# Kernel tuning notes

Measured on AMD Instinct MI355X. Metric: run time of the kernel, lower is better.

The kernel has to match this reference:

```python
import jax, jax.numpy as jnp
import numpy as np

N = 16384      # total ligand atoms
E = 65536      # edges
B = 256        # graphs / batch
MAXN = 64      # atoms per graph (max_nodes for to_dense_batch)
FIN = 64       # num_node_features
HID = 256      # hidden_channels
GH = 2         # gat heads
LP = 1024      # protein length
NH = 4         # cross-attention heads
HD = HID // NH
VOCAB = 22


def setup_inputs() -> dict:
    key = jax.random.key(0)
    ks = jax.random.split(key, 48)
    f = jnp.float32
    def nrm(k, shape, s=0.05):
        return jax.random.normal(k, shape, f) * s
    inp = {}
    inp["x"] = jax.random.normal(ks[0], (N, FIN), f)
    inp["edge_index"] = jax.random.randint(ks[1], (2, E), 0, N)
    inp["batch"] = jnp.arange(N) // MAXN  # sorted, 64 atoms per graph
    inp["protein_seq"] = jax.random.randint(ks[2], (B, LP), 0, VOCAB)
    # GAT layer 1 (FIN -> HID, GH heads, concat=False)
    inp["w1"] = nrm(ks[3], (FIN, GH * HID)); inp["as1"] = nrm(ks[4], (GH, HID)); inp["ad1"] = nrm(ks[5], (GH, HID)); inp["b1"] = jnp.zeros((HID,), f)
    inp["w2"] = nrm(ks[6], (HID, GH * HID)); inp["as2"] = nrm(ks[7], (GH, HID)); inp["ad2"] = nrm(ks[8], (GH, HID)); inp["b2"] = jnp.zeros((HID,), f)
    inp["w3"] = nrm(ks[9], (HID, GH * HID)); inp["as3"] = nrm(ks[10], (GH, HID)); inp["ad3"] = nrm(ks[11], (GH, HID)); inp["b3"] = jnp.zeros((HID,), f)
    # protein embedding + conv1d (OIH layout)
    inp["emb"] = nrm(ks[12], (VOCAB, HID), 0.1)
    inp["conv_w"] = nrm(ks[13], (HID, HID, 3)); inp["conv_b"] = jnp.zeros((HID,), f)
    # cross-attention MHA
    inp["wq"] = nrm(ks[14], (HID, HID)); inp["bq"] = jnp.zeros((HID,), f)
    inp["wk"] = nrm(ks[15], (HID, HID)); inp["bk"] = jnp.zeros((HID,), f)
    inp["wv"] = nrm(ks[16], (HID, HID)); inp["bv"] = jnp.zeros((HID,), f)
    inp["wo"] = nrm(ks[17], (HID, HID)); inp["bo"] = jnp.zeros((HID,), f)
    inp["ln1_g"] = jnp.ones((HID,), f); inp["ln1_b"] = jnp.zeros((HID,), f)
    inp["ffw1"] = nrm(ks[18], (HID, 4 * HID)); inp["ffb1"] = jnp.zeros((4 * HID,), f)
    inp["ffw2"] = nrm(ks[19], (4 * HID, HID)); inp["ffb2"] = jnp.zeros((HID,), f)
    inp["ln2_g"] = jnp.ones((HID,), f); inp["ln2_b"] = jnp.zeros((HID,), f)
    inp["fc1_w"] = nrm(ks[20], (HID, HID)); inp["fc1_b"] = jnp.zeros((HID,), f)
    inp["fc2_w"] = nrm(ks[21], (HID, 1)); inp["fc2_b"] = jnp.zeros((1,), f)
    return inp


def _gat(x, edge_index, W, a_src, a_dst, bias):
    # PyG GATConv, concat=False (mean over heads), add_self_loops=True
    n = x.shape[0]
    h = (x @ W).reshape(n, GH, HID)                      # [N,GH,C]
    loop = jnp.arange(n)
    src = jnp.concatenate([edge_index[0], loop])
    dst = jnp.concatenate([edge_index[1], loop])
    a_s = jnp.einsum('nhc,hc->nh', h, a_src)             # [N,GH]
    a_d = jnp.einsum('nhc,hc->nh', h, a_dst)
    e = jax.nn.leaky_relu(a_s[src] + a_d[dst], 0.2)      # [E+N,GH]
    emax = jax.ops.segment_max(e, dst, num_segments=n)   # each node has a self-loop
    ex = jnp.exp(e - emax[dst])
    den = jax.ops.segment_sum(ex, dst, num_segments=n)
    alpha = ex / den[dst]                                # [E+N,GH]
    msg = h[src] * alpha[:, :, None]
    out = jax.ops.segment_sum(msg, dst, num_segments=n)  # [N,GH,C]
    return out.mean(axis=1) + bias


def _to_dense_batch(x, batch):
    # batch is sorted node->graph ids; counts per graph <= MAXN
    ones = jnp.ones((x.shape[0],), jnp.int32)
    counts = jax.ops.segment_sum(ones, batch, num_segments=B)
    starts = jnp.cumsum(counts) - counts
    pos = jnp.arange(x.shape[0]) - starts[batch]
    dense = jnp.zeros((B, MAXN, x.shape[1]), x.dtype).at[batch, pos].set(x)
    mask = jnp.zeros((B, MAXN), bool).at[batch, pos].set(True)
    return dense, mask


def _layernorm(x, g, b, eps=1e-5):
    mu = x.mean(-1, keepdims=True)
    var = ((x - mu) ** 2).mean(-1, keepdims=True)
    return (x - mu) * jax.lax.rsqrt(var + eps) * g + b


def reference(x, edge_index, batch, protein_seq,
              w1, as1, ad1, b1, w2, as2, ad2, b2, w3, as3, ad3, b3,
              emb, conv_w, conv_b,
              wq, bq, wk, bk, wv, bv, wo, bo,
              ln1_g, ln1_b, ffw1, ffb1, ffw2, ffb2, ln2_g, ln2_b,
              fc1_w, fc1_b, fc2_w, fc2_b):
    # --- ligand GNN (eval mode: dropout = identity) ---
    h = jax.nn.elu(_gat(x, edge_index, w1, as1, ad1, b1))
    h = jax.nn.elu(_gat(h, edge_index, w2, as2, ad2, b2))
    h = jax.nn.elu(_gat(h, edge_index, w3, as3, ad3, b3))
    lig, lig_mask = _to_dense_batch(h, batch)            # [B,MAXN,HID], [B,MAXN]
    # --- protein branch ---
    p = emb[protein_seq]                                 # [B,LP,HID]
    p = p.transpose(0, 2, 1)                             # [B,HID,LP]
    p = jax.lax.conv_general_dilated(p, conv_w, (1,), [(1, 1)],
                                     dimension_numbers=('NCH', 'OIH', 'NCH'))
    p = jax.nn.relu(p + conv_b[None, :, None]).transpose(0, 2, 1)  # [B,LP,HID]
    kpm = protein_seq == 0                               # key padding mask
    # --- cross attention (query=ligand, key/value=protein) ---
    q = (lig @ wq + bq).reshape(B, MAXN, NH, HD)
    k = (p @ wk + bk).reshape(B, LP, NH, HD)
    v = (p @ wv + bv).reshape(B, LP, NH, HD)
    scores = jnp.einsum('bqhd,bkhd->bhqk', q, k) / np.sqrt(HD).astype(np.float32)
    scores = jnp.where(kpm[:, None, None, :], jnp.float32(-1e9), scores)
    attn = jax.nn.softmax(scores, axis=-1)               # [B,NH,MAXN,LP]
    ctx = jnp.einsum('bhqk,bkhd->bqhd', attn, v).reshape(B, MAXN, HID)
    attn_out = ctx @ wo + bo
    y = _layernorm(lig + attn_out, ln1_g, ln1_b)
    ff = jax.nn.gelu(y @ ffw1 + ffb1, approximate=False) @ ffw2 + ffb2
    y = _layernorm(y + ff, ln2_g, ln2_b)
    # --- masked mean pool ---
    m = lig_mask[:, :, None].astype(y.dtype)
    pooled = (y * m).sum(axis=1) / (m.sum(axis=1) + 1e-6)
    out = jax.nn.relu(pooled @ fc1_w + fc1_b)
    return out @ fc2_w + fc2_b                           # [B,1]
```

## Files before the change

kernel.cpp:

```cpp
#include <hip/hip_runtime.h>
#include <hip/hip_bf16.h>
#include <cstdint>
#include <cstddef>

#define NAT 16384
#define NED 65536
#define BGR 256
#define FIN 64
#define HID 256
#define LPN 1024
#define HD 64
#define NTRIP 11638
#define NTAB  11648

typedef __bf16 bf16x8 __attribute__((ext_vector_type(8)));
typedef float floatx4 __attribute__((ext_vector_type(4)));

__device__ __forceinline__ void gl2lds16(const void* g, void* l)
{
    __builtin_amdgcn_global_load_lds(
        (const __attribute__((address_space(1))) unsigned int*)g,
        (__attribute__((address_space(3))) unsigned int*)l, 16, 0, 0);
}

template<int ACT, int OUTBF16, int BIASROW, int HSPLIT>
__global__ __launch_bounds__(512) void gemm_mfma(const __bf16* __restrict__ A,
    const __bf16* __restrict__ Bt, const float* __restrict__ bias,
    void* __restrict__ Cout, int M, int Nn, int K, float escale)
{
    __shared__ __bf16 As[2][128][32];
    __shared__ __bf16 Bs[2][128][32];
    const int t = threadIdx.x;
    const int m0 = blockIdx.y * 128, n0 = blockIdx.x * 128;
    const int w = t >> 6, lane = t & 63;
    const int wm = (w & 3) * 32, wn = (w >> 2) * 64;
    const int quad = lane >> 4, l16 = lane & 15;
    const int r0 = t >> 2, s0 = t & 3, g0 = (s0 ^ (r0 & 3)) * 8;
    const int fso = (quad ^ (l16 & 3)) * 8;
    floatx4 acc[2][4] = {};
    for (int k0 = 0; k0 < K; k0 += 64) {
        gl2lds16(A + (size_t)(m0 + r0) * K + k0 + g0,       &As[0][r0][s0 * 8]);
        gl2lds16(A + (size_t)(m0 + r0) * K + k0 + 32 + g0,  &As[1][r0][s0 * 8]);
        gl2lds16(Bt + (size_t)(n0 + r0) * K + k0 + g0,      &Bs[0][r0][s0 * 8]);
        gl2lds16(Bt + (size_t)(n0 + r0) * K + k0 + 32 + g0, &Bs[1][r0][s0 * 8]);
        __syncthreads();
#pragma unroll
        for (int c = 0; c < 2; c++) {
            bf16x8 af[2], bfr[4];
#pragma unroll
            for (int mi = 0; mi < 2; mi++) af[mi]  = *(const bf16x8*)&As[c][wm + mi * 16 + l16][fso];
#pragma unroll
            for (int nj = 0; nj < 4; nj++) bfr[nj] = *(const bf16x8*)&Bs[c][wn + nj * 16 + l16][fso];
#pragma unroll
            for (int mi = 0; mi < 2; mi++)
#pragma unroll
                for (int nj = 0; nj < 4; nj++)
                    acc[mi][nj] = __builtin_amdgcn_mfma_f32_16x16x32_bf16(af[mi], bfr[nj], acc[mi][nj], 0, 0, 0);
        }
        __syncthreads();
    }
#pragma unroll
    for (int mi = 0; mi < 2; mi++)
#pragma unroll
        for (int nj = 0; nj < 4; nj++) {
            int col = n0 + wn + nj * 16 + l16;
#pragma unroll
            for (int r = 0; r < 4; r++) {
                int row = m0 + wm + mi * 16 + quad * 4 + r;
                float bval = bias ? (BIASROW ? bias[row] : bias[col]) : 0.f;
                float v = (acc[mi][nj][r] + bval) * escale;
                if (ACT == 1) v = fmaxf(v, 0.f);
                if (ACT == 2) v = 0.5f * v * (1.f + erff(v * 0.70710678118654752f));
                if (HSPLIT)      ((__bf16*)Cout)[((size_t)(col >> 6) * M + row) * 64 + (col & 63)] = (__bf16)v;
                else if (OUTBF16) ((__bf16*)Cout)[(size_t)row * Nn + col] = (__bf16)v;
                else              ((float*)Cout)[(size_t)row * Nn + col] = v;
            }
        }
}

__global__ __launch_bounds__(512) void gemm_gat(const __bf16* __restrict__ A,
    const __bf16* __restrict__ Bt, const float* __restrict__ as_f,
    const float* __restrict__ ad_f, __bf16* __restrict__ Hg,
    float* __restrict__ part, int K)
{
    __shared__ __bf16 As[2][128][32];
    __shared__ __bf16 Bs[2][128][32];
    const int t = threadIdx.x;
    const int m0 = blockIdx.y * 128, n0 = blockIdx.x * 128;
    const int w = t >> 6, lane = t & 63;
    const int wm = (w & 3) * 32, wn = (w >> 2) * 64;
    const int quad = lane >> 4, l16 = lane & 15;
    const int r0 = t >> 2, s0 = t & 3, g0 = (s0 ^ (r0 & 3)) * 8;
    const int fso = (quad ^ (l16 & 3)) * 8;
    floatx4 acc[2][4] = {};
    for (int k0 = 0; k0 < K; k0 += 64) {
        gl2lds16(A + (size_t)(m0 + r0) * K + k0 + g0,       &As[0][r0][s0 * 8]);
        gl2lds16(A + (size_t)(m0 + r0) * K + k0 + 32 + g0,  &As[1][r0][s0 * 8]);
        gl2lds16(Bt + (size_t)(n0 + r0) * K + k0 + g0,      &Bs[0][r0][s0 * 8]);
        gl2lds16(Bt + (size_t)(n0 + r0) * K + k0 + 32 + g0, &Bs[1][r0][s0 * 8]);
        __syncthreads();
#pragma unroll
        for (int c = 0; c < 2; c++) {
            bf16x8 af[2], bfr[4];
#pragma unroll
            for (int mi = 0; mi < 2; mi++) af[mi]  = *(const bf16x8*)&As[c][wm + mi * 16 + l16][fso];
#pragma unroll
            for (int nj = 0; nj < 4; nj++) bfr[nj] = *(const bf16x8*)&Bs[c][wn + nj * 16 + l16][fso];
#pragma unroll
            for (int mi = 0; mi < 2; mi++)
#pragma unroll
                for (int nj = 0; nj < 4; nj++)
                    acc[mi][nj] = __builtin_amdgcn_mfma_f32_16x16x32_bf16(af[mi], bfr[nj], acc[mi][nj], 0, 0, 0);
        }
        __syncthreads();
    }
    const int slot = blockIdx.x * 2 + (w >> 2);
#pragma unroll
    for (int mi = 0; mi < 2; mi++) {
#pragma unroll
        for (int r = 0; r < 4; r++) {
            float ps = 0.f, pd = 0.f;
#pragma unroll
            for (int nj = 0; nj < 4; nj++) {
                int col = n0 + wn + nj * 16 + l16;
                float v = acc[mi][nj][r];
                ps += v * as_f[col];
                pd += v * ad_f[col];
            }
#pragma unroll
            for (int off = 1; off < 16; off <<= 1) {
                ps += __shfl_xor(ps, off, 64);
                pd += __shfl_xor(pd, off, 64);
            }
            if (l16 == 0) {
                int row = m0 + wm + mi * 16 + quad * 4 + r;
                part[(size_t)(slot * 2 + 0) * NAT + row] = ps;
                part[(size_t)(slot * 2 + 1) * NAT + row] = pd;
            }
        }
    }
#pragma unroll
    for (int mi = 0; mi < 2; mi++)
#pragma unroll
        for (int nj = 0; nj < 4; nj++) {
            int col = n0 + wn + nj * 16 + l16;
#pragma unroll
            for (int r = 0; r < 4; r++) {
                int row = m0 + wm + mi * 16 + quad * 4 + r;
                Hg[(size_t)row * 512 + col] = (__bf16)acc[mi][nj][r];
            }
        }
}

__global__ void fold_k(const float* __restrict__ part, float* __restrict__ a_s,
                       float* __restrict__ a_d)
{
    int n = blockIdx.x * 256 + threadIdx.x;
    float s0 = 0.f, d0 = 0.f, s1 = 0.f, d1 = 0.f;
#pragma unroll
    for (int sl = 0; sl < 4; sl++) {
        s0 += part[(size_t)(sl * 2 + 0) * NAT + n];
        d0 += part[(size_t)(sl * 2 + 1) * NAT + n];
        s1 += part[(size_t)((sl + 4) * 2 + 0) * NAT + n];
        d1 += part[(size_t)((sl + 4) * 2 + 1) * NAT + n];
    }
    a_s[n * 2 + 0] = s0; a_s[n * 2 + 1] = s1;
    a_d[n * 2 + 0] = d0; a_d[n * 2 + 1] = d1;
}

__global__ __launch_bounds__(256) void tap_k(const float* __restrict__ emb,
    const float* __restrict__ cw, float* __restrict__ tap)
{
    const int dlv = blockIdx.x >> 2, part = blockIdx.x & 3;
    const int dl = dlv / 22, v = dlv % 22;
    const int n = threadIdx.x;
    const float* er = emb + v * 256 + part * 64;
    const float* wr = cw + (size_t)n * 768 + part * 192 + dl;
    float s = 0.f;
    for (int k = 0; k < 64; k += 4) {
        s += er[k + 0] * wr[k * 3 + 0];
        s += er[k + 1] * wr[k * 3 + 3];
        s += er[k + 2] * wr[k * 3 + 6];
        s += er[k + 3] * wr[k * 3 + 9];
    }
    atomicAdd(&tap[(size_t)dlv * 256 + n], s);
}

__global__ __launch_bounds__(256) void ptab_k(const float* __restrict__ tap,
    const float* __restrict__ bias, __bf16* __restrict__ P)
{
    const int t = threadIdx.x;
    const int row = blockIdx.x * 8 + (t >> 5);
    const int c = (t & 31) * 8;
    __bf16 o[8];
    if (row < NTRIP) {
        const int a = row / 506, rem = row - a * 506;
        const int t1 = rem / 23, c2 = rem - t1 * 23;
        float acc[8];
#pragma unroll
        for (int j = 0; j < 8; j++) acc[j] = bias[c + j];
        if (a > 0) {
            const float* r = tap + (size_t)(0 * 22 + (a - 1)) * 256 + c;
#pragma unroll
            for (int j = 0; j < 8; j++) acc[j] += r[j];
        }
        {
            const float* r = tap + (size_t)(1 * 22 + t1) * 256 + c;
#pragma unroll
            for (int j = 0; j < 8; j++) acc[j] += r[j];
        }
        if (c2 > 0) {
            const float* r = tap + (size_t)(2 * 22 + (c2 - 1)) * 256 + c;
#pragma unroll
            for (int j = 0; j < 8; j++) acc[j] += r[j];
        }
#pragma unroll
        for (int j = 0; j < 8; j++) o[j] = (__bf16)fmaxf(acc[j], 0.f);
    } else {
#pragma unroll
        for (int j = 0; j < 8; j++) o[j] = (__bf16)0.f;
    }
    *(uint4*)(P + (size_t)row * 256 + c) = *(uint4*)o;
}

__global__ void tid_k(const int* __restrict__ seq, unsigned short* __restrict__ tid)
{
    int i = blockIdx.x * 256 + threadIdx.x;
    int b = i >> 10, l = i & 1023;
    const int* sr = seq + b * LPN;
    int t0 = (l > 0) ? sr[l - 1] : -1;
    int t1 = sr[l];
    int t2 = (l < LPN - 1) ? sr[l + 1] : -1;
    int v = (t0 + 1) * 506 + t1 * 23 + (t2 + 1);
    tid[i] = (unsigned short)(v | (t1 == 0 ? 0x8000 : 0));
}

struct Segs {
    const float* src[12];
    __bf16* dst[12];
    int kdim[12];
    int ndim[12];
    int mode[12];
    int start[13];
};

__global__ void cvtall_k(Segs S, int total)
{
    int i = blockIdx.x * 256 + threadIdx.x;
    if (i >= total) return;
    int s = 0;
    while (i >= S.start[s + 1]) s++;
    int j = i - S.start[s];
    if (S.mode[s] == 0) {
        S.dst[s][j] = (__bf16)S.src[s][j];
    } else {
        int K = S.kdim[s], N = S.ndim[s];
        int n = j / K, k = j - n * K;
        S.dst[s][j] = (__bf16)S.src[s][(size_t)k * N + n];
    }
}

__global__ void deg_k(const int* __restrict__ ei, int* __restrict__ deg)
{
    int e = blockIdx.x * 256 + threadIdx.x;
    if (e < NED) atomicAdd(&deg[ei[NED + e]], 1);
}

__global__ __launch_bounds__(256) void scan_k(const int* __restrict__ deg, int* __restrict__ rowptr)
{
    __shared__ int part[256];
    int t = threadIdx.x;
    int base = t * 64;
    int s = 0;
#pragma unroll
    for (int i = 0; i < 64; i++) s += deg[base + i];
    part[t] = s;
    __syncthreads();
    for (int off = 1; off < 256; off <<= 1) {
        int v = (t >= off) ? part[t - off] : 0;
        __syncthreads();
        part[t] += v;
        __syncthreads();
    }
    int run = t ? part[t - 1] : 0;
    for (int i = 0; i < 64; i++) { rowptr[base + i] = run; run += deg[base + i]; }
    if (t == 255) rowptr[16384] = run;
}

__global__ void scat_k(const int* __restrict__ ei, int* __restrict__ fill,
                       const int* __restrict__ rowptr, int* __restrict__ csrc,
                       int* __restrict__ cdst)
{
    int e = blockIdx.x * 256 + threadIdx.x;
    if (e >= NED) return;
    int d = ei[NED + e];
    int pos = rowptr[d] + atomicAdd(&fill[d], 1);
    csrc[pos] = ei[e];
    cdst[pos] = d;
}

__global__ void erec_k(const int* __restrict__ csrc, const int* __restrict__ cdst,
    const float* __restrict__ a_s, const float* __restrict__ a_d,
    float4* __restrict__ rec)
{
    int p = blockIdx.x * 256 + threadIdx.x;
    if (p >= NED) return;
    int s = csrc[p], d = cdst[p];
    float2 as2 = *(const float2*)(a_s + s * 2);
    float2 ad2 = *(const float2*)(a_d + d * 2);
    float e0 = as2.x + ad2.x; e0 = (e0 > 0.f) ? e0 : 0.2f * e0;
    float e1 = as2.y + ad2.y; e1 = (e1 > 0.f) ? e1 : 0.2f * e1;
    rec[p] = make_float4(e0, e1, __int_as_float(s), 0.f);
}

__global__ __launch_bounds__(256) void gat_agg(const int* __restrict__ rowptr,
    const float4* __restrict__ rec, const __bf16* __restrict__ hgb,
    const float* __restrict__ a_s, const float* __restrict__ a_d,
    const float* __restrict__ bias, float* __restrict__ out, __bf16* __restrict__ outb)
{
    const int wave = threadIdx.x >> 6, lane = threadIdx.x & 63;
    const int d = blockIdx.x * 4 + wave;
    const int beg = rowptr[d], end = rowptr[d + 1];
    float2 as2 = *(const float2*)(a_s + d * 2);
    float2 ad2 = *(const float2*)(a_d + d * 2);
    float e0 = as2.x + ad2.x; e0 = (e0 > 0.f) ? e0 : 0.2f * e0;
    float e1 = as2.y + ad2.y; e1 = (e1 > 0.f) ? e1 : 0.2f * e1;
    float m0 = e0, den0 = 1.f, m1 = e1, den1 = 1.f;
    for (int p = beg; p < end; p++) {
        float4 rc = rec[p];
        float nm0 = fmaxf(m0, rc.x);
        den0 = den0 * __expf(m0 - nm0) + __expf(rc.x - nm0);
        m0 = nm0;
        float nm1 = fmaxf(m1, rc.y);
        den1 = den1 * __expf(m1 - nm1) + __expf(rc.y - nm1);
        m1 = nm1;
    }
    const float inv0 = 1.f / den0, inv1 = 1.f / den1;
    const int ch = lane * 8;
    const int g = ch >> 8;
    const float mg = g ? m1 : m0, invg = g ? inv1 : inv0;
    float acc[8] = {};
    {
        float al = __expf((g ? e1 : e0) - mg) * invg;
        bf16x8 hv = *(const bf16x8*)(hgb + (size_t)d * 512 + ch);
#pragma unroll
        for (int j = 0; j < 8; j++) acc[j] += (float)hv[j] * al;
    }
    for (int p = beg; p < end; p++) {
        float4 rc = rec[p];
        float al = __expf((g ? rc.y : rc.x) - mg) * invg;
        int s = __float_as_int(rc.z);
        bf16x8 hv = *(const bf16x8*)(hgb + (size_t)s * 512 + ch);
#pragma unroll
        for (int j = 0; j < 8; j++) acc[j] += (float)hv[j] * al;
    }
    float other[8];
#pragma unroll
    for (int j = 0; j < 8; j++) other[j] = __shfl_xor(acc[j], 32, 64);
    if (lane < 32) {
#pragma unroll
        for (int j = 0; j < 8; j++) {
            float v = 0.5f * (acc[j] + other[j]) + bias[ch + j];
            v = (v > 0.f) ? v : expm1f(v);
            if (out) out[(size_t)d * 256 + ch + j] = v;
            outb[(size_t)d * 256 + ch + j] = (__bf16)v;
        }
    }
}

__global__ __launch_bounds__(256, 4) void attn5_k(const __bf16* __restrict__ Qb,
    const __bf16* __restrict__ Ktab, const __bf16* __restrict__ Vtab,
    const unsigned short* __restrict__ tid16, __bf16* __restrict__ O)
{
    __shared__ __bf16 Vs[2][4096];
    __shared__ __bf16 Ps2[4][16][64];
    __shared__ float mask_f[1024];
    __shared__ unsigned short tids[1024];
    const int t = threadIdx.x;
    const int bid = blockIdx.x;
    const int h = (bid >> 1) & 3;
    const int b = ((bid >> 3) << 1) | (bid & 1);
    const int w = t >> 6, lane = t & 63;
    const int quad = lane >> 4, l16 = lane & 15;
    const int key = (l16 & 7) << 4;
    const __bf16* Kh = Ktab + (size_t)h * NTAB * 64;
    const __bf16* Vh = Vtab + (size_t)h * NTAB * 64;
    {
        const uint32_t* src = (const uint32_t*)(tid16 + (size_t)b * LPN);
        uint32_t v0 = src[t], v1 = src[t + 256];
        ((uint32_t*)tids)[t] = v0;
        ((uint32_t*)tids)[t + 256] = v1;
        mask_f[2 * t + 0] = (v0 & 0x8000u) ? -1e9f : 0.f;
        mask_f[2 * t + 1] = (v0 & 0x80000000u) ? -1e9f : 0.f;
        mask_f[2 * (t + 256) + 0] = (v1 & 0x8000u) ? -1e9f : 0.f;
        mask_f[2 * (t + 256) + 1] = (v1 & 0x80000000u) ? -1e9f : 0.f;
    }
    const __bf16* qrow = Qb + (size_t)(b * 64 + w * 16 + l16) * HID + h * HD;
    bf16x8 aq0 = *(const bf16x8*)(qrow + quad * 8);
    bf16x8 aq1 = *(const bf16x8*)(qrow + 32 + quad * 8);
    __syncthreads();

    auto loadV = [&](int kt, bf16x8* vr) {
#pragma unroll
        for (int it = 0; it < 2; it++) {
            const int ch0 = (w + it * 4) * 8;
            const int row = tids[kt * 64 + lane] & 0x7fff;
            vr[it] = *(const bf16x8*)(Vh + (size_t)row * 64 + ch0);
        }
    };
    auto writeV = [&](const bf16x8* vr, int buf) {
#pragma unroll
        for (int it = 0; it < 2; it++) {
            const int ch0 = (w + it * 4) * 8;
#pragma unroll
            for (int j = 0; j < 8; j++) {
                const int chl = ch0 + j;
                Vs[buf][chl * 64 + (((lane >> 3) ^ (chl & 7)) << 3) + (lane & 7)] = vr[it][j];
            }
        }
    };

    bf16x8 vr[2];
    loadV(0, vr);
    writeV(vr, 0);
    float m_run = -3e38f;
    float l_run = 0.f;
    floatx4 ctx[4] = {};
    __syncthreads();

    for (int kt = 0; kt < 16; kt++) {
        const int buf = kt & 1;
        const int kp0 = kt * 64;
        bf16x8 kc0[4], kc1[4];
#pragma unroll
        for (int nj = 0; nj < 4; nj++) {
            const int row = tids[kp0 + nj * 16 + l16] & 0x7fff;
            const __bf16* krow = Kh + (size_t)row * 64;
            kc0[nj] = *(const bf16x8*)(krow + quad * 8);
            kc1[nj] = *(const bf16x8*)(krow + 32 + quad * 8);
        }
        if (kt < 15) loadV(kt + 1, vr);
        floatx4 s[4];
#pragma unroll
        for (int nj = 0; nj < 4; nj++) {
            floatx4 z = {0.f, 0.f, 0.f, 0.f};
            s[nj] = __builtin_amdgcn_mfma_f32_16x16x32_bf16(kc0[nj], aq0, z, 0, 0, 0);
            s[nj] = __builtin_amdgcn_mfma_f32_16x16x32_bf16(kc1[nj], aq1, s[nj], 0, 0, 0);
        }
#pragma unroll
        for (int nj = 0; nj < 4; nj++) {
            floatx4 m4 = *(const floatx4*)&mask_f[kp0 + nj * 16 + quad * 4];
#pragma unroll
            for (int r = 0; r < 4; r++) s[nj][r] += m4[r];
        }
        float mx = -3e38f;
#pragma unroll
        for (int nj = 0; nj < 4; nj++)
#pragma unroll
            for (int r = 0; r < 4; r++) mx = fmaxf(mx, s[nj][r]);
        mx = fmaxf(mx, __shfl_xor(mx, 16, 64));
        mx = fmaxf(mx, __shfl_xor(mx, 32, 64));
        const float mn = fmaxf(m_run, mx);
        const float alpha = __expf(m_run - mn);
        m_run = mn;
        float rs = 0.f;
#pragma unroll
        for (int nj = 0; nj < 4; nj++)
#pragma unroll
            for (int r = 0; r < 4; r++) {
                float p = __expf(s[nj][r] - mn);
                s[nj][r] = p;
                rs += p;
            }
        rs += __shfl_xor(rs, 16, 64);
        rs += __shfl_xor(rs, 32, 64);
        l_run = l_run * alpha + rs;
        float al[4];
#pragma unroll
        for (int r = 0; r < 4; r++) al[r] = __shfl(alpha, quad * 4 + r, 64);
        {
            char* rowp = (char*)&Ps2[w][l16][0];
#pragma unroll
            for (int nj = 0; nj < 4; nj++) {
                union { uint2 u2; unsigned short us[4]; } pk;
#pragma unroll
                for (int r = 0; r < 4; r++) {
                    __bf16 bv = (__bf16)s[nj][r];
                    pk.us[r] = *(unsigned short*)&bv;
                }
                *(uint2*)(rowp + ((nj * 32 + quad * 8) ^ key)) = pk.u2;
            }
        }
        bf16x8 pa0 = *(const bf16x8*)((char*)&Ps2[w][l16][0] + ((quad * 16) ^ key));
        bf16x8 pa1 = *(const bf16x8*)((char*)&Ps2[w][l16][0] + ((64 + quad * 16) ^ key));
#pragma unroll
        for (int dj = 0; dj < 4; dj++) {
#pragma unroll
            for (int r = 0; r < 4; r++) ctx[dj][r] *= al[r];
            const int chl = dj * 16 + l16;
            bf16x8 bv0 = *(const bf16x8*)&Vs[buf][chl * 64 + ((quad ^ (chl & 7)) << 3)];
            bf16x8 bv1 = *(const bf16x8*)&Vs[buf][chl * 64 + (((quad + 4) ^ (chl & 7)) << 3)];
            ctx[dj] = __builtin_amdgcn_mfma_f32_16x16x32_bf16(pa0, bv0, ctx[dj], 0, 0, 0);
            ctx[dj] = __builtin_amdgcn_mfma_f32_16x16x32_bf16(pa1, bv1, ctx[dj], 0, 0, 0);
        }
        if (kt < 15) writeV(vr, buf ^ 1);
        __syncthreads();
    }
    float ll[4];
#pragma unroll
    for (int r = 0; r < 4; r++) ll[r] = __shfl(l_run, quad * 4 + r, 64);
#pragma unroll
    for (int dj = 0; dj < 4; dj++)
#pragma unroll
        for (int r = 0; r < 4; r++) {
            int q = w * 16 + quad * 4 + r;
            O[((size_t)(b * 64 + q)) * 256 + h * HD + dj * 16 + l16] = (__bf16)(ctx[dj][r] / ll[r]);
        }
}

__device__ __forceinline__ float blockSum256(float v, float* red)
{
#pragma unroll
    for (int off = 32; off >= 1; off >>= 1) v += __shfl_down(v, off, 64);
    int wave = threadIdx.x >> 6, lane = threadIdx.x & 63;
    if (lane == 0) red[wave] = v;
    __syncthreads();
    float s = red[0] + red[1] + red[2] + red[3];
    __syncthreads();
    return s;
}

__global__ __launch_bounds__(256) void lnres_k(const float* __restrict__ A,
    const float* __restrict__ Bb, const float* __restrict__ g,
    const float* __restrict__ be, float* __restrict__ Y, __bf16* __restrict__ Yb)
{
    __shared__ float red[4];
    int r = blockIdx.x, t = threadIdx.x;
    float v = A[(size_t)r * 256 + t] + Bb[(size_t)r * 256 + t];
    float mean = blockSum256(v, red) * (1.f / 256.f);
    float d = v - mean;
    float var = blockSum256(d * d, red) * (1.f / 256.f);
    float o = d * rsqrtf(var + 1e-5f) * g[t] + be[t];
    Y[(size_t)r * 256 + t] = o;
    if (Yb) Yb[(size_t)r * 256 + t] = (__bf16)o;
}

__global__ __launch_bounds__(256) void head_k(const float* __restrict__ Y,
    const float* __restrict__ fc1w, const float* __restrict__ fc1b,
    const float* __restrict__ fc2w, const float* __restrict__ fc2b,
    float* __restrict__ out)
{
    __shared__ float pooled[256];
    __shared__ float h[256];
    __shared__ float red[4];
    int b = blockIdx.x, t = threadIdx.x;
    float s = 0.f;
#pragma unroll 8
    for (int q = 0; q < 64; q++) s += Y[(size_t)(b * 64 + q) * 256 + t];
    pooled[t] = s / (64.f + 1e-6f);
    __syncthreads();
    float a = 0.f;
    for (int k = 0; k < 256; k += 4) {
        a += pooled[k + 0] * fc1w[(k + 0) * 256 + t];
        a += pooled[k + 1] * fc1w[(k + 1) * 256 + t];
        a += pooled[k + 2] * fc1w[(k + 2) * 256 + t];
        a += pooled[k + 3] * fc1w[(k + 3) * 256 + t];
    }
    h[t] = fmaxf(a + fc1b[t], 0.f);
    __syncthreads();
    float p = h[t] * fc2w[t];
    p = blockSum256(p, red);
    if (t == 0) out[b] = p + fc2b[0];
}

extern "C" void kernel_launch(void* const* d_in, const int* in_sizes, int n_in,
                              void* d_out, int out_size, void* d_ws, size_t ws_size,
                              hipStream_t stream)
{
    const float* x     = (const float*)d_in[0];
    const int*   ei    = (const int*)d_in[1];
    const int*   pseq  = (const int*)d_in[3];
    const float* w1  = (const float*)d_in[4];
    const float* as1 = (const float*)d_in[5];
    const float* ad1 = (const float*)d_in[6];
    const float* b1  = (const float*)d_in[7];
    const float* w2  = (const float*)d_in[8];
    const float* as2 = (const float*)d_in[9];
    const float* ad2 = (const float*)d_in[10];
    const float* b2  = (const float*)d_in[11];
    const float* w3  = (const float*)d_in[12];
    const float* as3 = (const float*)d_in[13];
    const float* ad3 = (const float*)d_in[14];
    const float* b3  = (const float*)d_in[15];
    const float* emb    = (const float*)d_in[16];
    const float* conv_w = (const float*)d_in[17];
    const float* conv_b = (const float*)d_in[18];
    const float* wq = (const float*)d_in[19];
    const float* bq = (const float*)d_in[20];
    const float* wk = (const float*)d_in[21];
    const float* bk = (const float*)d_in[22];
    const float* wv = (const float*)d_in[23];
    const float* bv = (const float*)d_in[24];
    const float* wo = (const float*)d_in[25];
    const float* bo = (const float*)d_in[26];
    const float* ln1_g = (const float*)d_in[27];
    const float* ln1_b = (const float*)d_in[28];
    const float* ffw1  = (const float*)d_in[29];
    const float* ffb1  = (const float*)d_in[30];
    const float* ffw2  = (const float*)d_in[31];
    const float* ffb2  = (const float*)d_in[32];
    const float* ln2_g = (const float*)d_in[33];
    const float* ln2_b = (const float*)d_in[34];
    const float* fc1_w = (const float*)d_in[35];
    const float* fc1_b = (const float*)d_in[36];
    const float* fc2_w = (const float*)d_in[37];
    const float* fc2_b = (const float*)d_in[38];
    (void)in_sizes; (void)n_in; (void)out_size;

    char* ws = (char*)d_ws;
    size_t off = 0;
    auto alloc = [&](size_t bytes) -> char* {
        char* p = ws + off;
        off += (bytes + 255) & ~(size_t)255;
        return p;
    };
    __bf16* hgb  = (__bf16*)alloc((size_t)NAT * 512 * 2);
    float* og    = (float*)alloc((size_t)NAT * 512 * 4);
    float* hb0   = (float*)alloc((size_t)NAT * 256 * 4);
    float* hb1   = (float*)alloc((size_t)NAT * 256 * 4);
    __bf16* xb   = (__bf16*)alloc((size_t)NAT * FIN * 2);
    __bf16* hbb  = (__bf16*)alloc((size_t)NAT * 256 * 2);
    __bf16* qbb  = (__bf16*)alloc((size_t)NAT * 256 * 2);
    __bf16* ctxbb= (__bf16*)alloc((size_t)NAT * 256 * 2);
    __bf16* ybb  = (__bf16*)alloc((size_t)NAT * 256 * 2);
    float* a_s   = (float*)alloc((size_t)NAT * 2 * 4);
    float* a_d   = (float*)alloc((size_t)NAT * 2 * 4);
    float* asd_p = (float*)alloc((size_t)16 * NAT * 4);
    int* deg     = (int*)alloc((size_t)NAT * 4);
    int* fill    = (int*)alloc((size_t)NAT * 4);
    int* rowptr  = (int*)alloc((size_t)(NAT + 1) * 4);
    int* csrc    = (int*)alloc((size_t)NED * 4);
    int* cdst    = (int*)alloc((size_t)NED * 4);
    float4* erec = (float4*)alloc((size_t)NED * 16);
    float* tap   = (float*)alloc((size_t)3 * 22 * 256 * 4);
    __bf16* ptab = (__bf16*)alloc((size_t)NTAB * 256 * 2);
    __bf16* Ktab = (__bf16*)alloc((size_t)NTAB * 256 * 2);
    __bf16* Vtab = (__bf16*)alloc((size_t)NTAB * 256 * 2);
    unsigned short* tid16 = (unsigned short*)alloc((size_t)BGR * LPN * 2);
    __bf16* w1T  = (__bf16*)alloc((size_t)512 * 64 * 2);
    __bf16* w2T  = (__bf16*)alloc((size_t)512 * 256 * 2);
    __bf16* w3T  = (__bf16*)alloc((size_t)512 * 256 * 2);
    __bf16* wkT  = (__bf16*)alloc((size_t)256 * 256 * 2);
    __bf16* wvT  = (__bf16*)alloc((size_t)256 * 256 * 2);
    __bf16* wqT  = (__bf16*)alloc((size_t)256 * 256 * 2);
    __bf16* woT  = (__bf16*)alloc((size_t)256 * 256 * 2);
    __bf16* f1T  = (__bf16*)alloc((size_t)1024 * 256 * 2);
    __bf16* f2T  = (__bf16*)alloc((size_t)256 * 1024 * 2);
    size_t fixed_end = off;
    char* region   = ws + fixed_end;
    __bf16* ffbb   = (__bf16*)region;
    float*  y2     = (float*)(region + (size_t)NAT * 1024 * 2);
    float* attno = og;
    float* ybuf  = og + (size_t)NAT * 256;
    float* ff2o  = hb1;
    (void)ws_size;

    hipMemsetAsync(deg, 0, (size_t)NAT * 8, stream);
    hipMemsetAsync(tap, 0, (size_t)3 * 22 * 256 * 4, stream);
    deg_k<<<NED / 256, 256, 0, stream>>>(ei, deg);
    scan_k<<<1, 256, 0, stream>>>(deg, rowptr);
    scat_k<<<NED / 256, 256, 0, stream>>>(ei, fill, rowptr, csrc, cdst);
    tap_k<<<264, 256, 0, stream>>>(emb, conv_w, tap);

    {
        Segs S;
        const float* srcs[10] = {x, w1, w2, w3, wk, wv, wq, wo, ffw1, ffw2};
        __bf16* dsts[10] = {xb, w1T, w2T, w3T, wkT, wvT, wqT, woT, f1T, f2T};
        int kd[10] = {0, 64, 256, 256, 256, 256, 256, 256, 256, 1024};
        int nd[10] = {0, 512, 512, 512, 256, 256, 256, 256, 1024, 256};
        int md[10] = {0, 1, 1, 1, 1, 1, 1, 1, 1, 1};
        int cnt[10] = {NAT * FIN, 32768, 131072, 131072,
                       65536, 65536, 65536, 65536, 262144, 262144};
        int run = 0;
        for (int i = 0; i < 10; i++) {
            S.src[i] = srcs[i]; S.dst[i] = dsts[i];
            S.kdim[i] = kd[i]; S.ndim[i] = nd[i]; S.mode[i] = md[i];
            S.start[i] = run; run += cnt[i];
        }
        S.start[10] = run; S.start[11] = run; S.start[12] = run;
        cvtall_k<<<(run + 255) / 256, 256, 0, stream>>>(S, run);
    }

    ptab_k<<<NTAB / 8, 256, 0, stream>>>(tap, conv_b, ptab);
    tid_k<<<BGR * LPN / 256, 256, 0, stream>>>(pseq, tid16);
    gemm_mfma<0, 1, 0, 1><<<dim3(2, NTAB / 128), 512, 0, stream>>>(ptab, wkT, bk, Ktab, NTAB, 256, 256, 1.f);
    gemm_mfma<0, 1, 0, 1><<<dim3(2, NTAB / 128), 512, 0, stream>>>(ptab, wvT, bv, Vtab, NTAB, 256, 256, 1.f);

    const __bf16* WT[3] = {w1T, w2T, w3T};
    const float* asl[3] = {as1, as2, as3};
    const float* adl[3] = {ad1, ad2, ad3};
    const float* bl[3]  = {b1, b2, b3};
    float* houts[3] = {nullptr, nullptr, hb0};
    const __bf16* hinb = xb;
    int Kdim = FIN;
    for (int l = 0; l < 3; l++) {
        gemm_gat<<<dim3(4, NAT / 128), 512, 0, stream>>>(hinb, WT[l], asl[l], adl[l], hgb, asd_p, Kdim);
        fold_k<<<NAT / 256, 256, 0, stream>>>(asd_p, a_s, a_d);
        erec_k<<<NED / 256, 256, 0, stream>>>(csrc, cdst, a_s, a_d, erec);
        gat_agg<<<NAT / 4, 256, 0, stream>>>(rowptr, erec, hgb, a_s, a_d, bl[l], houts[l], hbb);
        hinb = hbb;
        Kdim = HID;
    }
    const float* lig = hb0;
    const __bf16* ligb = hbb;

    gemm_mfma<0, 1, 0, 0><<<dim3(2, NAT / 128), 512, 0, stream>>>(ligb, wqT, bq, qbb, NAT, 256, 256, 0.125f);

    attn5_k<<<BGR * 4, 256, 0, stream>>>(qbb, Ktab, Vtab, tid16, ctxbb);

    gemm_mfma<0, 0, 0, 0><<<dim3(2, NAT / 128), 512, 0, stream>>>(ctxbb, woT, bo, attno, NAT, 256, 256, 1.f);
    lnres_k<<<NAT, 256, 0, stream>>>(lig, attno, ln1_g, ln1_b, ybuf, ybb);
    gemm_mfma<2, 1, 0, 0><<<dim3(8, NAT / 128), 512, 0, stream>>>(ybb, f1T, ffb1, ffbb, NAT, 1024, 256, 1.f);
    gemm_mfma<0, 0, 0, 0><<<dim3(2, NAT / 128), 512, 0, stream>>>(ffbb, f2T, ffb2, ff2o, NAT, 256, 1024, 1.f);
    lnres_k<<<NAT, 256, 0, stream>>>(ybuf, ff2o, ln2_g, ln2_b, y2, nullptr);

    head_k<<<BGR, 256, 0, stream>>>(y2, fc1_w, fc1_b, fc2_w, fc2_b, (float*)d_out);
}
```

Measured before the change: 536.3 us.

## Stage K tiles into LDS via async global_load_lds and single-buffer V

The attention kernel now loads each 64-key K tile into double-buffered shared memory with direct global-to-LDS loads, using an XOR swizzle. Each wave then reads K fragments from LDS instead of issuing scattered per-lane gathers from global memory. V moves to a single LDS buffer with a new coalesced load pattern and a different swizzle. This costs an extra barrier per iteration before the V write. The aim is to cut redundant global K traffic across the four waves and overlap the next K tile's load with compute.

```diff
diff --git a/kernel.cpp b/kernel.cpp
--- a/kernel.cpp
+++ b/kernel.cpp
@@ -368,11 +368,12 @@
     }
 }
 
-__global__ __launch_bounds__(256, 4) void attn5_k(const __bf16* __restrict__ Qb,
+__global__ __launch_bounds__(256, 4) void attn6_k(const __bf16* __restrict__ Qb,
     const __bf16* __restrict__ Ktab, const __bf16* __restrict__ Vtab,
     const unsigned short* __restrict__ tid16, __bf16* __restrict__ O)
 {
-    __shared__ __bf16 Vs[2][4096];
+    __shared__ __bf16 Ks[2][4096];
+    __shared__ __bf16 Vs[4096];
     __shared__ __bf16 Ps2[4][16][64];
     __shared__ float mask_f[1024];
     __shared__ unsigned short tids[1024];
@@ -400,29 +401,43 @@
     bf16x8 aq1 = *(const bf16x8*)(qrow + 32 + quad * 8);
     __syncthreads();
 
-    auto loadV = [&](int kt, bf16x8* vr) {
+    auto stageK = [&](int kt, int bufb) {
 #pragma unroll
         for (int it = 0; it < 2; it++) {
-            const int ch0 = (w + it * 4) * 8;
-            const int row = tids[kt * 64 + lane] & 0x7fff;
-            vr[it] = *(const bf16x8*)(Vh + (size_t)row * 64 + ch0);
+            const int s = it * 256 + t;
+            const int pos = s >> 3;
+            const int c = (s & 7) ^ (pos & 7);
+            const int row = tids[kt * 64 + pos] & 0x7fff;
+            gl2lds16(Kh + (size_t)row * 64 + c * 8,
+                     &Ks[bufb][(it * 256 + w * 64) * 8]);
         }
     };
-    auto writeV = [&](const bf16x8* vr, int buf) {
+    auto loadV = [&](int kt, bf16x8* vrr) {
 #pragma unroll
         for (int it = 0; it < 2; it++) {
-            const int ch0 = (w + it * 4) * 8;
+            const int pos = w * 8 + (lane >> 3) + it * 32;
+            const int row = tids[kt * 64 + pos] & 0x7fff;
+            vrr[it] = *(const bf16x8*)(Vh + (size_t)row * 64 + (lane & 7) * 8);
+        }
+    };
+    auto writeV = [&](const bf16x8* vrr) {
+        const int p = lane >> 3, c = lane & 7;
+#pragma unroll
+        for (int it = 0; it < 2; it++) {
+            const int pos = w * 8 + p + it * 32;
+            const int cp = pos >> 3;
 #pragma unroll
             for (int j = 0; j < 8; j++) {
-                const int chl = ch0 + j;
-                Vs[buf][chl * 64 + (((lane >> 3) ^ (chl & 7)) << 3) + (lane & 7)] = vr[it][j];
+                const int chl = c * 8 + j;
+                Vs[chl * 64 + (((cp ^ c ^ j) & 7) << 3) + p] = vrr[it][j];
             }
         }
     };
 
     bf16x8 vr[2];
+    stageK(0, 0);
     loadV(0, vr);
-    writeV(vr, 0);
+    writeV(vr);
     float m_run = -3e38f;
     float l_run = 0.f;
     floatx4 ctx[4] = {};
@@ -431,21 +446,21 @@
     for (int kt = 0; kt < 16; kt++) {
         const int buf = kt & 1;
         const int kp0 = kt * 64;
-        bf16x8 kc0[4], kc1[4];
+        if (kt < 15) {
+            stageK(kt + 1, buf ^ 1);
+            loadV(kt + 1, vr);
+        }
+        const int ksl0 = (quad ^ (l16 & 7)) * 8;
+        const int ksl1 = ((quad + 4) ^ (l16 & 7)) * 8;
+        floatx4 s[4];
 #pragma unroll
         for (int nj = 0; nj < 4; nj++) {
-            const int row = tids[kp0 + nj * 16 + l16] & 0x7fff;
-            const __bf16* krow = Kh + (size_t)row * 64;
-            kc0[nj] = *(const bf16x8*)(krow + quad * 8);
-            kc1[nj] = *(const bf16x8*)(krow + 32 + quad * 8);
-        }
-        if (kt < 15) loadV(kt + 1, vr);
-        floatx4 s[4];
-#pragma unroll
-        for (int nj = 0; nj < 4; nj++) {
+            const __bf16* kr = &Ks[buf][(nj * 16 + l16) * 64];
+            bf16x8 k0 = *(const bf16x8*)&kr[ksl0];
+            bf16x8 k1 = *(const bf16x8*)&kr[ksl1];
             floatx4 z = {0.f, 0.f, 0.f, 0.f};
-            s[nj] = __builtin_amdgcn_mfma_f32_16x16x32_bf16(kc0[nj], aq0, z, 0, 0, 0);
-            s[nj] = __builtin_amdgcn_mfma_f32_16x16x32_bf16(kc1[nj], aq1, s[nj], 0, 0, 0);
+            s[nj] = __builtin_amdgcn_mfma_f32_16x16x32_bf16(k0, aq0, z, 0, 0, 0);
+            s[nj] = __builtin_amdgcn_mfma_f32_16x16x32_bf16(k1, aq1, s[nj], 0, 0, 0);
         }
 #pragma unroll
         for (int nj = 0; nj < 4; nj++) {
@@ -498,12 +513,14 @@
 #pragma unroll
             for (int r = 0; r < 4; r++) ctx[dj][r] *= al[r];
             const int chl = dj * 16 + l16;
-            bf16x8 bv0 = *(const bf16x8*)&Vs[buf][chl * 64 + ((quad ^ (chl & 7)) << 3)];
-            bf16x8 bv1 = *(const bf16x8*)&Vs[buf][chl * 64 + (((quad + 4) ^ (chl & 7)) << 3)];
+            const int Xc = ((chl >> 3) ^ (chl & 7)) & 7;
+            bf16x8 bv0 = *(const bf16x8*)&Vs[chl * 64 + (((quad ^ Xc) & 7) << 3)];
+            bf16x8 bv1 = *(const bf16x8*)&Vs[chl * 64 + ((((quad + 4) ^ Xc) & 7) << 3)];
             ctx[dj] = __builtin_amdgcn_mfma_f32_16x16x32_bf16(pa0, bv0, ctx[dj], 0, 0, 0);
             ctx[dj] = __builtin_amdgcn_mfma_f32_16x16x32_bf16(pa1, bv1, ctx[dj], 0, 0, 0);
         }
-        if (kt < 15) writeV(vr, buf ^ 1);
+        __syncthreads();
+        if (kt < 15) writeV(vr);
         __syncthreads();
     }
     float ll[4];
@@ -716,7 +733,7 @@
 
     gemm_mfma<0, 1, 0, 0><<<dim3(2, NAT / 128), 512, 0, stream>>>(ligb, wqT, bq, qbb, NAT, 256, 256, 0.125f);
 
-    attn5_k<<<BGR * 4, 256, 0, stream>>>(qbb, Ktab, Vtab, tid16, ctxbb);
+    attn6_k<<<BGR * 4, 256, 0, stream>>>(qbb, Ktab, Vtab, tid16, ctxbb);
 
     gemm_mfma<0, 0, 0, 0><<<dim3(2, NAT / 128), 512, 0, stream>>>(ctxbb, woT, bo, attno, NAT, 256, 256, 1.f);
     lnres_k<<<NAT, 256, 0, stream>>>(lig, attno, ln1_g, ln1_b, ybuf, ybb);
```

Result: faster. 505.4 us (-5.8%).
